# Kernel optimization log

Hardware: AMD Instinct MI355X
Metric: run time of the kernel (lower is better)

The kernel has to match this reference:

```python
import jax, jax.numpy as jnp
import numpy as np

B, N, F, R, DEG, STEPS = 4, 1024, 128, 16, 16, 2


def setup_inputs() -> dict:
    key = jax.random.key(0)
    ks = jax.random.split(key, 12)
    BN = B * N
    E = BN * DEG

    def edges(k):
        # edges kept within each graph of size N, then offset per graph
        e = jax.random.randint(k, (2, E), 0, N)
        off = jnp.repeat(jnp.arange(B, dtype=jnp.int32) * N, N * DEG)
        return e + off[None, :]

    return {
        "x_s": jax.random.normal(ks[0], (BN, F), jnp.float32),
        "edge_index_s": edges(ks[1]),
        "x_t": jax.random.normal(ks[2], (BN, F), jnp.float32),
        "edge_index_t": edges(ks[3]),
        "W1_self": jax.random.normal(ks[4], (F, F), jnp.float32) / np.float32(np.sqrt(F)),
        "W1_nbr": jax.random.normal(ks[5], (F, F), jnp.float32) / np.float32(np.sqrt(F)),
        "b1": jnp.zeros((F,), jnp.float32),
        "W2_self": jax.random.normal(ks[6], (R, R), jnp.float32) / np.float32(np.sqrt(R)),
        "W2_nbr": jax.random.normal(ks[7], (R, R), jnp.float32) / np.float32(np.sqrt(R)),
        "b2": jnp.zeros((R,), jnp.float32),
        "Wm1": jax.random.normal(ks[8], (R, R), jnp.float32) / np.float32(np.sqrt(R)),
        "bm1": jnp.zeros((R,), jnp.float32),
        "Wm2": jax.random.normal(ks[9], (R, 1), jnp.float32) / np.float32(np.sqrt(R)),
        "bm2": jnp.zeros((1,), jnp.float32),
        "r_steps": jax.random.normal(ks[10], (STEPS, B, N, R), jnp.float32),
    }


def _psi(x, ei, Ws, Wn, b):
    # simple GraphConv: self transform + summed neighbor transform
    agg = jax.ops.segment_sum(x[ei[0]], ei[1], num_segments=x.shape[0])
    return jax.nn.relu(x @ Ws + agg @ Wn + b)


def reference(x_s, edge_index_s, x_t, edge_index_t, W1_self, W1_nbr, b1,
              W2_self, W2_nbr, b2, Wm1, bm1, Wm2, bm2, r_steps):
    # psi_1 on both graphs, then dense-batch to [B, N, F] (equal-size graphs,
    # so masks are all-True and masked_softmax == softmax)
    h_s = _psi(x_s, edge_index_s, W1_self, W1_nbr, b1).reshape(B, N, F)
    h_t = _psi(x_t, edge_index_t, W1_self, W1_nbr, b1).reshape(B, N, F)

    S_hat = jnp.einsum('bsf,btf->bst', h_s, h_t)  # [B, Ns, Nt]
    S_0 = jax.nn.softmax(S_hat, axis=-1)

    for i in range(STEPS):
        S = jax.nn.softmax(S_hat, axis=-1)
        r_s = r_steps[i]                             # [B, N, R]
        r_t = jnp.einsum('bst,bsr->btr', S, r_s)     # S^T @ r_s
        o_s = _psi(r_s.reshape(B * N, R), edge_index_s, W2_self, W2_nbr, b2).reshape(B, N, R)
        o_t = _psi(r_t.reshape(B * N, R), edge_index_t, W2_self, W2_nbr, b2).reshape(B, N, R)
        D = o_s[:, :, None, :] - o_t[:, None, :, :]  # [B, Ns, Nt, R]
        upd = (jax.nn.relu(D @ Wm1 + bm1) @ Wm2 + bm2)[..., 0]
        S_hat = S_hat + upd

    S_L = jax.nn.softmax(S_hat, axis=-1)
    return (S_0, S_L)
```

## Files before the change

### kernel.cpp

```cpp
#include <hip/hip_runtime.h>

#define B_ 4
#define N_ 1024
#define F_ 128
#define R_ 16
#define E_ 65536
#define BN_ 4096

__global__ __launch_bounds__(256) void hist_k(
    const int* __restrict__ eis, const int* __restrict__ eit, int* __restrict__ counts) {
  const int* ei = blockIdx.y ? eit : eis;
  int* c = counts + blockIdx.y * BN_;
  int e = blockIdx.x * 256 + threadIdx.x;
  atomicAdd(c + ei[E_ + e], 1);
}

__global__ __launch_bounds__(256) void csr_scan(
    const int* __restrict__ counts, int* __restrict__ offs, int* __restrict__ cursor) {
  const int* c = counts + blockIdx.x * BN_;
  int* o = offs + blockIdx.x * (BN_ + 1);
  int* cur = cursor + blockIdx.x * BN_;
  int tid = threadIdx.x;
  int base = tid * 16;
  int local[16], sum = 0;
#pragma unroll
  for (int i = 0; i < 16; i++) { local[i] = sum; sum += c[base + i]; }
  __shared__ int csum[256];
  csum[tid] = sum;
  __syncthreads();
  for (int d = 1; d < 256; d <<= 1) {
    int v = (tid >= d) ? csum[tid - d] : 0;
    __syncthreads();
    csum[tid] += v;
    __syncthreads();
  }
  int prev = (tid == 0) ? 0 : csum[tid - 1];
#pragma unroll
  for (int i = 0; i < 16; i++) { int off = prev + local[i]; o[base + i] = off; cur[base + i] = off; }
  if (tid == 255) o[BN_] = csum[255];
}

__global__ __launch_bounds__(256) void csr_fill(
    const int* __restrict__ eis, const int* __restrict__ eit,
    int* __restrict__ cursor, int* __restrict__ csr) {
  const int* ei = blockIdx.y ? eit : eis;
  int* cur = cursor + blockIdx.y * BN_;
  int* cs = csr + blockIdx.y * E_;
  int e = blockIdx.x * 256 + threadIdx.x;
  int src = ei[e], dst = ei[E_ + e];
  int pos = atomicAdd(cur + dst, 1);
  cs[pos] = src;
}

__global__ __launch_bounds__(256) void gather_f(
    const float* __restrict__ xs, const float* __restrict__ xt,
    const int* __restrict__ csr, const int* __restrict__ offs,
    float* __restrict__ aggs, float* __restrict__ aggt) {
  const float* x = blockIdx.y ? xt : xs;
  const int* cs = csr + blockIdx.y * E_;
  const int* of = offs + blockIdx.y * (BN_ + 1);
  float* agg = blockIdx.y ? aggt : aggs;
  int node = blockIdx.x * 2 + (threadIdx.x >> 7);
  int ch = threadIdx.x & 127;
  int j0 = of[node], j1 = of[node + 1];
  float a0 = 0.f, a1 = 0.f, a2 = 0.f, a3 = 0.f;
  int j = j0;
  for (; j + 3 < j1; j += 4) {
    int s0 = cs[j], s1 = cs[j + 1], s2 = cs[j + 2], s3 = cs[j + 3];
    a0 += x[(size_t)s0 * F_ + ch];
    a1 += x[(size_t)s1 * F_ + ch];
    a2 += x[(size_t)s2 * F_ + ch];
    a3 += x[(size_t)s3 * F_ + ch];
  }
  for (; j < j1; j++) a0 += x[(size_t)cs[j] * F_ + ch];
  agg[(size_t)node * F_ + ch] = (a0 + a1) + (a2 + a3);
}

__global__ __launch_bounds__(256) void psi1_gemm(
    const float* __restrict__ xs, const float* __restrict__ aggs,
    const float* __restrict__ xt, const float* __restrict__ aggt,
    const float* __restrict__ Ws, const float* __restrict__ Wn,
    const float* __restrict__ bias, float* __restrict__ hs, float* __restrict__ ht) {
  const float* x   = blockIdx.z ? xt   : xs;
  const float* agg = blockIdx.z ? aggt : aggs;
  float*       h   = blockIdx.z ? ht   : hs;
  int n0 = blockIdx.x * 64, m0 = blockIdx.y * 64;
  int tid = threadIdx.x, tx = tid & 15, ty = tid >> 4;
  __shared__ __align__(16) float sA[16][68];
  __shared__ __align__(16) float sB[16][68];
  float acc[4][4] = {};
  for (int phase = 0; phase < 2; phase++) {
    const float* A  = phase ? agg : x;
    const float* Bw = phase ? Wn  : Ws;
    for (int kb = 0; kb < F_; kb += 16) {
      int row = tid >> 2, k4 = (tid & 3) * 4;
      float4 va = *(const float4*)(A + (size_t)(m0 + row) * F_ + kb + k4);
      sA[k4 + 0][row] = va.x; sA[k4 + 1][row] = va.y;
      sA[k4 + 2][row] = va.z; sA[k4 + 3][row] = va.w;
      int k = tid >> 4, n4 = (tid & 15) * 4;
      *(float4*)&sB[k][n4] = *(const float4*)(Bw + (size_t)(kb + k) * F_ + n0 + n4);
      __syncthreads();
#pragma unroll
      for (int kk = 0; kk < 16; kk++) {
        float a[4], bb[4];
        *(float4*)a  = *(const float4*)&sA[kk][ty * 4];
        *(float4*)bb = *(const float4*)&sB[kk][tx * 4];
#pragma unroll
        for (int i = 0; i < 4; i++)
#pragma unroll
          for (int j = 0; j < 4; j++) acc[i][j] += a[i] * bb[j];
      }
      __syncthreads();
    }
  }
  float4 bv = *(const float4*)(bias + n0 + tx * 4);
  float bj[4] = {bv.x, bv.y, bv.z, bv.w};
#pragma unroll
  for (int i = 0; i < 4; i++) {
    int m = m0 + ty * 4 + i;
    float4 o;
    o.x = fmaxf(acc[i][0] + bj[0], 0.f); o.y = fmaxf(acc[i][1] + bj[1], 0.f);
    o.z = fmaxf(acc[i][2] + bj[2], 0.f); o.w = fmaxf(acc[i][3] + bj[3], 0.f);
    *(float4*)(h + (size_t)m * F_ + n0 + tx * 4) = o;
  }
}

__global__ __launch_bounds__(256) void shat_gemm(
    const float* __restrict__ hs, const float* __restrict__ ht, float* __restrict__ S) {
  int b = blockIdx.z;
  int n0 = blockIdx.x * 128, m0 = blockIdx.y * 128;
  int tid = threadIdx.x, tx = tid & 15, ty = tid >> 4;
  __shared__ __align__(16) float sA[16][132];
  __shared__ __align__(16) float sB[16][132];
  float acc[8][8] = {};
  const float* Ag = hs + (size_t)(b * N_ + m0) * F_;
  const float* Bg = ht + (size_t)(b * N_ + n0) * F_;
  for (int kb = 0; kb < F_; kb += 16) {
#pragma unroll
    for (int l = 0; l < 2; l++) {
      int idx = tid + l * 256;
      int row = idx >> 2, k4 = (idx & 3) * 4;
      float4 va = *(const float4*)(Ag + (size_t)row * F_ + kb + k4);
      sA[k4 + 0][row] = va.x; sA[k4 + 1][row] = va.y;
      sA[k4 + 2][row] = va.z; sA[k4 + 3][row] = va.w;
      float4 vb = *(const float4*)(Bg + (size_t)row * F_ + kb + k4);
      sB[k4 + 0][row] = vb.x; sB[k4 + 1][row] = vb.y;
      sB[k4 + 2][row] = vb.z; sB[k4 + 3][row] = vb.w;
    }
    __syncthreads();
#pragma unroll
    for (int kk = 0; kk < 16; kk++) {
      float a[8], bb[8];
      *(float4*)&a[0]  = *(const float4*)&sA[kk][ty * 8];
      *(float4*)&a[4]  = *(const float4*)&sA[kk][ty * 8 + 4];
      *(float4*)&bb[0] = *(const float4*)&sB[kk][tx * 8];
      *(float4*)&bb[4] = *(const float4*)&sB[kk][tx * 8 + 4];
#pragma unroll
      for (int i = 0; i < 8; i++)
#pragma unroll
        for (int j = 0; j < 8; j++) acc[i][j] += a[i] * bb[j];
    }
    __syncthreads();
  }
#pragma unroll
  for (int i = 0; i < 8; i++) {
    size_t off = ((size_t)(b * N_ + m0 + ty * 8 + i)) * N_ + n0 + tx * 8;
    float4 o0 = {acc[i][0], acc[i][1], acc[i][2], acc[i][3]};
    float4 o1 = {acc[i][4], acc[i][5], acc[i][6], acc[i][7]};
    *(float4*)(S + off) = o0; *(float4*)(S + off + 4) = o1;
  }
}

__global__ __launch_bounds__(256) void softmax_row(
    const float* __restrict__ in, float* __restrict__ out) {
  int row = blockIdx.x;
  float4 v = ((const float4*)(in + (size_t)row * N_))[threadIdx.x];
  float m = fmaxf(fmaxf(v.x, v.y), fmaxf(v.z, v.w));
#pragma unroll
  for (int o = 32; o > 0; o >>= 1) m = fmaxf(m, __shfl_down(m, o, 64));
  __shared__ float rmax[4], rsum[4];
  int wave = threadIdx.x >> 6, lane = threadIdx.x & 63;
  if (lane == 0) rmax[wave] = m;
  __syncthreads();
  m = fmaxf(fmaxf(rmax[0], rmax[1]), fmaxf(rmax[2], rmax[3]));
  float e0 = __expf(v.x - m), e1 = __expf(v.y - m);
  float e2 = __expf(v.z - m), e3 = __expf(v.w - m);
  float s = e0 + e1 + e2 + e3;
#pragma unroll
  for (int o = 32; o > 0; o >>= 1) s += __shfl_down(s, o, 64);
  if (lane == 0) rsum[wave] = s;
  __syncthreads();
  s = rsum[0] + rsum[1] + rsum[2] + rsum[3];
  float inv = 1.f / s;
  float4 o4 = {e0 * inv, e1 * inv, e2 * inv, e3 * inv};
  ((float4*)(out + (size_t)row * N_))[threadIdx.x] = o4;
}

__global__ __launch_bounds__(256) void row_stats(
    const float* __restrict__ in, float2* __restrict__ stats) {
  int row = blockIdx.x;
  float4 v = ((const float4*)(in + (size_t)row * N_))[threadIdx.x];
  float m = fmaxf(fmaxf(v.x, v.y), fmaxf(v.z, v.w));
#pragma unroll
  for (int o = 32; o > 0; o >>= 1) m = fmaxf(m, __shfl_down(m, o, 64));
  __shared__ float rmax[4], rsum[4];
  int wave = threadIdx.x >> 6, lane = threadIdx.x & 63;
  if (lane == 0) rmax[wave] = m;
  __syncthreads();
  m = fmaxf(fmaxf(rmax[0], rmax[1]), fmaxf(rmax[2], rmax[3]));
  float s = __expf(v.x - m) + __expf(v.y - m) + __expf(v.z - m) + __expf(v.w - m);
#pragma unroll
  for (int o = 32; o > 0; o >>= 1) s += __shfl_down(s, o, 64);
  if (lane == 0) rsum[wave] = s;
  __syncthreads();
  if (threadIdx.x == 0) {
    float tot = rsum[0] + rsum[1] + rsum[2] + rsum[3];
    stats[row] = make_float2(m, 1.f / tot);
  }
}

template <bool EXP>
__global__ __launch_bounds__(256) void rt_part_k(
    const float* __restrict__ S, const float2* __restrict__ stats,
    const float* __restrict__ rs, float* __restrict__ part) {
  int b = blockIdx.z, c = blockIdx.y, t0 = blockIdx.x * 256;
  int tid = threadIdx.x;
  int s0 = c * 32;
  __shared__ float rsh[32][16];
  __shared__ float sstat[64];
  if (tid < 128) {
    int srow = tid >> 2, c4 = (tid & 3) * 4;
    float4 v = *(const float4*)(rs + ((size_t)(b * N_ + s0 + srow)) * R_ + c4);
    rsh[srow][c4] = v.x; rsh[srow][c4 + 1] = v.y;
    rsh[srow][c4 + 2] = v.z; rsh[srow][c4 + 3] = v.w;
  } else if (EXP && tid < 192) {
    sstat[tid - 128] = ((const float*)(stats + b * N_ + s0))[tid - 128];
  }
  __syncthreads();
  float acc[16] = {};
  const float* Sp = S + ((size_t)(b * N_ + s0)) * N_ + t0 + tid;
#pragma unroll
  for (int s = 0; s < 32; s++) {
    float sv = Sp[(size_t)s * N_];
    if (EXP) sv = __expf(sv - sstat[2 * s]) * sstat[2 * s + 1];
#pragma unroll
    for (int r = 0; r < 16; r++) acc[r] += sv * rsh[s][r];
  }
  float* o = part + ((size_t)((b * 32 + c) * N_) + t0 + tid) * R_;
  *(float4*)(o + 0)  = *(float4*)&acc[0];
  *(float4*)(o + 4)  = *(float4*)&acc[4];
  *(float4*)(o + 8)  = *(float4*)&acc[8];
  *(float4*)(o + 12) = *(float4*)&acc[12];
}

__global__ __launch_bounds__(256) void rt_reduce(
    const float* __restrict__ part, float* __restrict__ rt) {
  int gid = blockIdx.x * 256 + threadIdx.x;
  int b = gid >> 12, tr = gid & 4095;
  const float* p = part + (size_t)b * (32 * N_ * R_) + (size_t)tr * 4;
  float4 acc = {0.f, 0.f, 0.f, 0.f};
#pragma unroll
  for (int c = 0; c < 32; c++) {
    float4 v = *(const float4*)(p + (size_t)c * (N_ * R_));
    acc.x += v.x; acc.y += v.y; acc.z += v.z; acc.w += v.w;
  }
  ((float4*)rt)[gid] = acc;
}

__global__ __launch_bounds__(256) void gpsi2p(
    const float* __restrict__ vs, const float* __restrict__ vt,
    const int* __restrict__ csr, const int* __restrict__ offs,
    const float* __restrict__ W2s, const float* __restrict__ W2n,
    const float* __restrict__ b2, const float* __restrict__ Wm1,
    float* __restrict__ Ps, float* __restrict__ Pt) {
  const float* v = blockIdx.y ? vt : vs;
  const int* cs = csr + blockIdx.y * E_;
  const int* of = offs + blockIdx.y * (BN_ + 1);
  float* P = blockIdx.y ? Pt : Ps;
  int col = threadIdx.x & 15, row = threadIdx.x >> 4;
  int node = blockIdx.x * 16 + row;
  int j0 = of[node], j1 = of[node + 1];
  float a0 = 0.f, a1 = 0.f, a2 = 0.f, a3 = 0.f;
  int j = j0;
  for (; j + 3 < j1; j += 4) {
    int s0 = cs[j], s1 = cs[j + 1], s2 = cs[j + 2], s3 = cs[j + 3];
    a0 += v[(size_t)s0 * R_ + col];
    a1 += v[(size_t)s1 * R_ + col];
    a2 += v[(size_t)s2 * R_ + col];
    a3 += v[(size_t)s3 * R_ + col];
  }
  for (; j < j1; j++) a0 += v[(size_t)cs[j] * R_ + col];
  __shared__ float sWs[16][16], sWn[16][16], sWm[16][17];
  __shared__ float sv[16][17], sa[16][17], so[16][17];
  sWs[row][col] = W2s[row * 16 + col];
  sWn[row][col] = W2n[row * 16 + col];
  sWm[row][col] = Wm1[row * 16 + col];
  sv[row][col] = v[(size_t)node * R_ + col];
  sa[row][col] = (a0 + a1) + (a2 + a3);
  __syncthreads();
  float o = b2[col];
#pragma unroll
  for (int k = 0; k < 16; k++) o += sv[row][k] * sWs[k][col] + sa[row][k] * sWn[k][col];
  so[row][col] = fmaxf(o, 0.f);
  __syncthreads();
  float p = 0;
#pragma unroll
  for (int k = 0; k < 16; k++) p += so[row][k] * sWm[k][col];
  P[(size_t)node * R_ + col] = p;
}

__global__ __launch_bounds__(256) void upd_kernel(
    float* __restrict__ Shat, const float* __restrict__ Ps, const float* __restrict__ Pt,
    const float* __restrict__ bm1, const float* __restrict__ Wm2,
    const float* __restrict__ bm2) {
  int b = blockIdx.z, s0 = blockIdx.y * 4, t0 = blockIdx.x * 256;
  int tid = threadIdx.x;
  __shared__ float pt[256][17];
  __shared__ float ps[4][16];
  __shared__ float sb[16], sw[16];
  for (int i = tid; i < 1024; i += 256) {
    int tr = i >> 2, c = (i & 3) * 4;
    const float4 v = *(const float4*)(Pt + ((size_t)(b * N_ + t0 + tr)) * R_ + c);
    pt[tr][c] = v.x; pt[tr][c + 1] = v.y; pt[tr][c + 2] = v.z; pt[tr][c + 3] = v.w;
  }
  if (tid < 64) ps[tid >> 4][tid & 15] = Ps[((size_t)(b * N_ + s0 + (tid >> 4))) * R_ + (tid & 15)];
  if (tid < 16) { sb[tid] = bm1[tid]; sw[tid] = Wm2[tid]; }
  __syncthreads();
  float bm2v = bm2[0];
  float ptl[16];
#pragma unroll
  for (int r = 0; r < 16; r++) ptl[r] = pt[tid][r];
#pragma unroll
  for (int si = 0; si < 4; si++) {
    size_t off = ((size_t)(b * N_ + s0 + si)) * N_ + t0 + tid;
    float sum = bm2v;
#pragma unroll
    for (int r = 0; r < 16; r++) sum += fmaxf(ps[si][r] - ptl[r] + sb[r], 0.f) * sw[r];
    Shat[off] += sum;
  }
}

extern "C" void kernel_launch(void* const* d_in, const int* in_sizes, int n_in,
                              void* d_out, int out_size, void* d_ws, size_t ws_size,
                              hipStream_t stream) {
  const float* x_s = (const float*)d_in[0];
  const int*   ei_s = (const int*)d_in[1];
  const float* x_t = (const float*)d_in[2];
  const int*   ei_t = (const int*)d_in[3];
  const float* W1s = (const float*)d_in[4];
  const float* W1n = (const float*)d_in[5];
  const float* b1  = (const float*)d_in[6];
  const float* W2s = (const float*)d_in[7];
  const float* W2n = (const float*)d_in[8];
  const float* b2  = (const float*)d_in[9];
  const float* Wm1 = (const float*)d_in[10];
  const float* bm1 = (const float*)d_in[11];
  const float* Wm2 = (const float*)d_in[12];
  const float* bm2 = (const float*)d_in[13];
  const float* r_steps = (const float*)d_in[14];

  float* out = (float*)d_out;
  float* S0 = out;
  float* SL = out + (size_t)B_ * N_ * N_;

  float* ws = (float*)d_ws;
  float* agg_s = ws;
  float* agg_t = ws + 524288;
  float* h_s   = ws + 1048576;
  float* h_t   = ws + 1572864;
  float* part  = ws;
  float* Shat  = ws + 2097152;
  float* rtb   = ws + 6291456;
  float2* stats = (float2*)(ws + 6356992);
  float* Ps    = ws + 6488064;
  float* Pt    = ws + 6553600;
  int* counts  = (int*)(ws + 6619136);
  int* cursor  = (int*)(ws + 6627328);
  int* offs    = (int*)(ws + 6635520);
  int* csr     = (int*)(ws + 6643720);

  hipMemsetAsync(counts, 0, 2 * BN_ * sizeof(int), stream);
  hist_k<<<dim3(E_ / 256, 2), 256, 0, stream>>>(ei_s, ei_t, counts);
  csr_scan<<<2, 256, 0, stream>>>(counts, offs, cursor);
  csr_fill<<<dim3(E_ / 256, 2), 256, 0, stream>>>(ei_s, ei_t, cursor, csr);

  gather_f<<<dim3(BN_ / 2, 2), 256, 0, stream>>>(x_s, x_t, csr, offs, agg_s, agg_t);
  psi1_gemm<<<dim3(2, 64, 2), 256, 0, stream>>>(x_s, agg_s, x_t, agg_t, W1s, W1n, b1, h_s, h_t);

  shat_gemm<<<dim3(8, 8, 4), 256, 0, stream>>>(h_s, h_t, Shat);
  softmax_row<<<B_ * N_, 256, 0, stream>>>(Shat, S0);

  for (int step = 0; step < 2; step++) {
    const float* rs = r_steps + (size_t)step * B_ * N_ * R_;
    if (step == 0) {
      rt_part_k<false><<<dim3(4, 32, 4), 256, 0, stream>>>(S0, nullptr, rs, part);
    } else {
      row_stats<<<B_ * N_, 256, 0, stream>>>(Shat, stats);
      rt_part_k<true><<<dim3(4, 32, 4), 256, 0, stream>>>(Shat, stats, rs, part);
    }
    rt_reduce<<<64, 256, 0, stream>>>(part, rtb);
    gpsi2p<<<dim3(256, 2), 256, 0, stream>>>(rs, rtb, csr, offs, W2s, W2n, b2, Wm1, Ps, Pt);
    upd_kernel<<<dim3(4, 256, 4), 256, 0, stream>>>(Shat, Ps, Pt, bm1, Wm2, bm2);
  }

  softmax_row<<<B_ * N_, 256, 0, stream>>>(Shat, SL);
}
```

Baseline: 257.0 us.

## Fuse row softmax stats into update kernel and build CSR in one block

The update kernel now owns whole rows: each block processes 4 source rows across all 1024 targets. It computes the softmax max and sum in registers, so the separate row_stats pass is gone and the final step writes S_L directly without re-reading Shat. CSR construction (histogram, scan, fill) is merged into a single kernel per graph using shared-memory atomics, which removes the memset and three launches. In exchange, the CSR build runs on only 2 blocks, serialising 64K edges per block, and the update grid is smaller with more registers per thread.

Measured after the change: 337.3 us. 1.31x slower.

```diff
diff --git a/kernel.cpp b/kernel.cpp
--- a/kernel.cpp
+++ b/kernel.cpp
@@ -7,49 +7,41 @@
 #define E_ 65536
 #define BN_ 4096
 
-__global__ __launch_bounds__(256) void hist_k(
-    const int* __restrict__ eis, const int* __restrict__ eit, int* __restrict__ counts) {
-  const int* ei = blockIdx.y ? eit : eis;
-  int* c = counts + blockIdx.y * BN_;
-  int e = blockIdx.x * 256 + threadIdx.x;
-  atomicAdd(c + ei[E_ + e], 1);
-}
-
-__global__ __launch_bounds__(256) void csr_scan(
-    const int* __restrict__ counts, int* __restrict__ offs, int* __restrict__ cursor) {
-  const int* c = counts + blockIdx.x * BN_;
-  int* o = offs + blockIdx.x * (BN_ + 1);
-  int* cur = cursor + blockIdx.x * BN_;
+__global__ __launch_bounds__(1024) void csr_build(
+    const int* __restrict__ eis, const int* __restrict__ eit,
+    int* __restrict__ offs, int* __restrict__ csr) {
+  int g = blockIdx.x;
+  const int* ei = g ? eit : eis;
+  int* o = offs + g * (BN_ + 1);
+  int* cs = csr + g * E_;
   int tid = threadIdx.x;
-  int base = tid * 16;
-  int local[16], sum = 0;
-#pragma unroll
-  for (int i = 0; i < 16; i++) { local[i] = sum; sum += c[base + i]; }
-  __shared__ int csum[256];
-  csum[tid] = sum;
-  __syncthreads();
-  for (int d = 1; d < 256; d <<= 1) {
-    int v = (tid >= d) ? csum[tid - d] : 0;
-    __syncthreads();
-    csum[tid] += v;
-    __syncthreads();
-  }
-  int prev = (tid == 0) ? 0 : csum[tid - 1];
-#pragma unroll
-  for (int i = 0; i < 16; i++) { int off = prev + local[i]; o[base + i] = off; cur[base + i] = off; }
-  if (tid == 255) o[BN_] = csum[255];
-}
-
-__global__ __launch_bounds__(256) void csr_fill(
-    const int* __restrict__ eis, const int* __restrict__ eit,
-    int* __restrict__ cursor, int* __restrict__ csr) {
-  const int* ei = blockIdx.y ? eit : eis;
-  int* cur = cursor + blockIdx.y * BN_;
-  int* cs = csr + blockIdx.y * E_;
-  int e = blockIdx.x * 256 + threadIdx.x;
-  int src = ei[e], dst = ei[E_ + e];
-  int pos = atomicAdd(cur + dst, 1);
-  cs[pos] = src;
+  __shared__ int cnt[BN_];
+  __shared__ int ssum[1024];
+  for (int i = tid; i < BN_; i += 1024) cnt[i] = 0;
+  __syncthreads();
+  for (int e = tid; e < E_; e += 1024) atomicAdd(&cnt[ei[E_ + e]], 1);
+  __syncthreads();
+  int base = tid * 4;
+  int c0 = cnt[base], c1 = cnt[base + 1], c2 = cnt[base + 2], c3 = cnt[base + 3];
+  ssum[tid] = c0 + c1 + c2 + c3;
+  __syncthreads();
+  for (int d = 1; d < 1024; d <<= 1) {
+    int v = (tid >= d) ? ssum[tid - d] : 0;
+    __syncthreads();
+    ssum[tid] += v;
+    __syncthreads();
+  }
+  int prev = (tid == 0) ? 0 : ssum[tid - 1];
+  int o0 = prev, o1 = o0 + c0, o2 = o1 + c1, o3 = o2 + c2;
+  o[base] = o0; o[base + 1] = o1; o[base + 2] = o2; o[base + 3] = o3;
+  if (tid == 1023) o[BN_] = ssum[1023];
+  cnt[base] = o0; cnt[base + 1] = o1; cnt[base + 2] = o2; cnt[base + 3] = o3;
+  __syncthreads();
+  for (int e = tid; e < E_; e += 1024) {
+    int src = ei[e], dst = ei[E_ + e];
+    int pos = atomicAdd(&cnt[dst], 1);
+    cs[pos] = src;
+  }
 }
 
 __global__ __launch_bounds__(256) void gather_f(
@@ -196,29 +188,6 @@
   ((float4*)(out + (size_t)row * N_))[threadIdx.x] = o4;
 }
 
-__global__ __launch_bounds__(256) void row_stats(
-    const float* __restrict__ in, float2* __restrict__ stats) {
-  int row = blockIdx.x;
-  float4 v = ((const float4*)(in + (size_t)row * N_))[threadIdx.x];
-  float m = fmaxf(fmaxf(v.x, v.y), fmaxf(v.z, v.w));
-#pragma unroll
-  for (int o = 32; o > 0; o >>= 1) m = fmaxf(m, __shfl_down(m, o, 64));
-  __shared__ float rmax[4], rsum[4];
-  int wave = threadIdx.x >> 6, lane = threadIdx.x & 63;
-  if (lane == 0) rmax[wave] = m;
-  __syncthreads();
-  m = fmaxf(fmaxf(rmax[0], rmax[1]), fmaxf(rmax[2], rmax[3]));
-  float s = __expf(v.x - m) + __expf(v.y - m) + __expf(v.z - m) + __expf(v.w - m);
-#pragma unroll
-  for (int o = 32; o > 0; o >>= 1) s += __shfl_down(s, o, 64);
-  if (lane == 0) rsum[wave] = s;
-  __syncthreads();
-  if (threadIdx.x == 0) {
-    float tot = rsum[0] + rsum[1] + rsum[2] + rsum[3];
-    stats[row] = make_float2(m, 1.f / tot);
-  }
-}
-
 template <bool EXP>
 __global__ __launch_bounds__(256) void rt_part_k(
     const float* __restrict__ S, const float2* __restrict__ stats,
@@ -309,34 +278,83 @@
   P[(size_t)node * R_ + col] = p;
 }
 
-__global__ __launch_bounds__(256) void upd_kernel(
+template <int LAST>
+__global__ __launch_bounds__(256) void upd_row(
     float* __restrict__ Shat, const float* __restrict__ Ps, const float* __restrict__ Pt,
     const float* __restrict__ bm1, const float* __restrict__ Wm2,
-    const float* __restrict__ bm2) {
-  int b = blockIdx.z, s0 = blockIdx.y * 4, t0 = blockIdx.x * 256;
+    const float* __restrict__ bm2, float2* __restrict__ stats, float* __restrict__ SL) {
+  int b = blockIdx.y, s0 = blockIdx.x * 4;
   int tid = threadIdx.x;
-  __shared__ float pt[256][17];
+  __shared__ __align__(16) float pt[256][17];
   __shared__ float ps[4][16];
   __shared__ float sb[16], sw[16];
-  for (int i = tid; i < 1024; i += 256) {
-    int tr = i >> 2, c = (i & 3) * 4;
-    const float4 v = *(const float4*)(Pt + ((size_t)(b * N_ + t0 + tr)) * R_ + c);
-    pt[tr][c] = v.x; pt[tr][c + 1] = v.y; pt[tr][c + 2] = v.z; pt[tr][c + 3] = v.w;
-  }
+  __shared__ float wred[4][4];
   if (tid < 64) ps[tid >> 4][tid & 15] = Ps[((size_t)(b * N_ + s0 + (tid >> 4))) * R_ + (tid & 15)];
   if (tid < 16) { sb[tid] = bm1[tid]; sw[tid] = Wm2[tid]; }
-  __syncthreads();
   float bm2v = bm2[0];
-  float ptl[16];
-#pragma unroll
-  for (int r = 0; r < 16; r++) ptl[r] = pt[tid][r];
+  float vals[4][4];
+  for (int tile = 0; tile < 4; tile++) {
+    int t0 = tile * 256;
+    __syncthreads();
+    for (int i = tid; i < 1024; i += 256) {
+      int tr = i >> 2, c = (i & 3) * 4;
+      float4 v = *(const float4*)(Pt + ((size_t)(b * N_ + t0 + tr)) * R_ + c);
+      pt[tr][c] = v.x; pt[tr][c + 1] = v.y; pt[tr][c + 2] = v.z; pt[tr][c + 3] = v.w;
+    }
+    __syncthreads();
+    float ptl[16];
+#pragma unroll
+    for (int r = 0; r < 16; r++) ptl[r] = pt[tid][r];
+#pragma unroll
+    for (int si = 0; si < 4; si++) {
+      size_t off = ((size_t)(b * N_ + s0 + si)) * N_ + t0 + tid;
+      float sum = bm2v;
+#pragma unroll
+      for (int r = 0; r < 16; r++) sum += fmaxf(ps[si][r] - ptl[r] + sb[r], 0.f) * sw[r];
+      float vv = Shat[off] + sum;
+      vals[tile][si] = vv;
+      if (!LAST) Shat[off] = vv;
+    }
+  }
+  int wave = tid >> 6, lane = tid & 63;
+  float M[4];
 #pragma unroll
   for (int si = 0; si < 4; si++) {
-    size_t off = ((size_t)(b * N_ + s0 + si)) * N_ + t0 + tid;
-    float sum = bm2v;
-#pragma unroll
-    for (int r = 0; r < 16; r++) sum += fmaxf(ps[si][r] - ptl[r] + sb[r], 0.f) * sw[r];
-    Shat[off] += sum;
+    float mm = fmaxf(fmaxf(vals[0][si], vals[1][si]), fmaxf(vals[2][si], vals[3][si]));
+#pragma unroll
+    for (int o = 32; o > 0; o >>= 1) mm = fmaxf(mm, __shfl_down(mm, o, 64));
+    if (lane == 0) wred[wave][si] = mm;
+  }
+  __syncthreads();
+#pragma unroll
+  for (int si = 0; si < 4; si++)
+    M[si] = fmaxf(fmaxf(wred[0][si], wred[1][si]), fmaxf(wred[2][si], wred[3][si]));
+  __syncthreads();
+  float L[4];
+#pragma unroll
+  for (int si = 0; si < 4; si++) {
+    float ls = __expf(vals[0][si] - M[si]) + __expf(vals[1][si] - M[si]) +
+               __expf(vals[2][si] - M[si]) + __expf(vals[3][si] - M[si]);
+#pragma unroll
+    for (int o = 32; o > 0; o >>= 1) ls += __shfl_down(ls, o, 64);
+    if (lane == 0) wred[wave][si] = ls;
+  }
+  __syncthreads();
+#pragma unroll
+  for (int si = 0; si < 4; si++)
+    L[si] = (wred[0][si] + wred[1][si]) + (wred[2][si] + wred[3][si]);
+  if (LAST) {
+#pragma unroll
+    for (int si = 0; si < 4; si++) {
+      float inv = 1.f / L[si];
+#pragma unroll
+      for (int tile = 0; tile < 4; tile++) {
+        size_t off = ((size_t)(b * N_ + s0 + si)) * N_ + tile * 256 + tid;
+        SL[off] = __expf(vals[tile][si] - M[si]) * inv;
+      }
+    }
+  } else {
+    if (tid < 4) stats[b * N_ + s0 + tid] = make_float2(M[tid], 1.f / L[tid]);
   }
 }
 
@@ -374,15 +392,10 @@
   float2* stats = (float2*)(ws + 6356992);
   float* Ps    = ws + 6488064;
   float* Pt    = ws + 6553600;
-  int* counts  = (int*)(ws + 6619136);
-  int* cursor  = (int*)(ws + 6627328);
-  int* offs    = (int*)(ws + 6635520);
-  int* csr     = (int*)(ws + 6643720);
-
-  hipMemsetAsync(counts, 0, 2 * BN_ * sizeof(int), stream);
-  hist_k<<<dim3(E_ / 256, 2), 256, 0, stream>>>(ei_s, ei_t, counts);
-  csr_scan<<<2, 256, 0, stream>>>(counts, offs, cursor);
-  csr_fill<<<dim3(E_ / 256, 2), 256, 0, stream>>>(ei_s, ei_t, cursor, csr);
+  int* offs    = (int*)(ws + 6619136);
+  int* csr     = (int*)(ws + 6627332);
+
+  csr_build<<<2, 1024, 0, stream>>>(ei_s, ei_t, offs, csr);
 
   gather_f<<<dim3(BN_ / 2, 2), 256, 0, stream>>>(x_s, x_t, csr, offs, agg_s, agg_t);
   psi1_gemm<<<dim3(2, 64, 2), 256, 0, stream>>>(x_s, agg_s, x_t, agg_t, W1s, W1n, b1, h_s, h_t);
@@ -390,18 +403,15 @@
   shat_gemm<<<dim3(8, 8, 4), 256, 0, stream>>>(h_s, h_t, Shat);
   softmax_row<<<B_ * N_, 256, 0, stream>>>(Shat, S0);
 
-  for (int step = 0; step < 2; step++) {
-    const float* rs = r_steps + (size_t)step * B_ * N_ * R_;
-    if (step == 0) {
-      rt_part_k<false><<<dim3(4, 32, 4), 256, 0, stream>>>(S0, nullptr, rs, part);
-    } else {
-      row_stats<<<B_ * N_, 256, 0, stream>>>(Shat, stats);
-      rt_part_k<true><<<dim3(4, 32, 4), 256, 0, stream>>>(Shat, stats, rs, part);
-    }
-    rt_reduce<<<64, 256, 0, stream>>>(part, rtb);
-    gpsi2p<<<dim3(256, 2), 256, 0, stream>>>(rs, rtb, csr, offs, W2s, W2n, b2, Wm1, Ps, Pt);
-    upd_kernel<<<dim3(4, 256, 4), 256, 0, stream>>>(Shat, Ps, Pt, bm1, Wm2, bm2);
-  }
-
-  softmax_row<<<B_ * N_, 256, 0, stream>>>(Shat, SL);
-}
+  const float* rs0 = r_steps;
+  rt_part_k<false><<<dim3(4, 32, 4), 256, 0, stream>>>(S0, nullptr, rs0, part);
+  rt_reduce<<<64, 256, 0, stream>>>(part, rtb);
+  gpsi2p<<<dim3(256, 2), 256, 0, stream>>>(rs0, rtb, csr, offs, W2s, W2n, b2, Wm1, Ps, Pt);
+  upd_row<0><<<dim3(256, 4), 256, 0, stream>>>(Shat, Ps, Pt, bm1, Wm2, bm2, stats, nullptr);
+
+  const float* rs1 = r_steps + (size_t)B_ * N_ * R_;
+  rt_part_k<true><<<dim3(4, 32, 4), 256, 0, stream>>>(Shat, stats, rs1, part);
+  rt_reduce<<<64, 256, 0, stream>>>(part, rtb);
+  gpsi2p<<<dim3(256, 2), 256, 0, stream>>>(rs1, rtb, csr, offs, W2s, W2n, b2, Wm1, Ps, Pt);
+  upd_row<1><<<dim3(256, 4), 256, 0, stream>>>(Shat, Ps, Pt, bm1, Wm2, bm2, nullptr, SL);
+}
```
